# Kernel optimization log

Hardware: AMD Instinct MI355X
Metric: run time of the kernel (lower is better)

Reference implementation:

```python
import jax, jax.numpy as jnp
import numpy as np

# Model dims
B, S, H, E, I, K = 2, 2048, 1024, 8, 1024, 2
ALPHA, LIMIT = 1.702, 7.0  # gpt_oss activation constants (module defaults)


def setup_inputs() -> dict:
    key = jax.random.key(0)
    ks = jax.random.split(key, 5)
    sc = 0.02
    return {
        "hidden_states": jax.random.normal(ks[0], (B, S, H), jnp.float32),
        "router_weight": jax.random.normal(ks[1], (H, E), jnp.float32) * sc,
        "gate_up_proj": jax.random.normal(ks[2], (E, H, 2 * I), jnp.float32) * sc,
        "gate_up_proj_bias": jnp.zeros((E, 2 * I), jnp.float32),
        "down_proj": jax.random.normal(ks[3], (E, I, H), jnp.float32) * sc,
        "down_proj_bias": jnp.zeros((E, H), jnp.float32),
    }


def reference(hidden_states, router_weight, gate_up_proj, gate_up_proj_bias,
              down_proj, down_proj_bias):
    Bt, St, Ht = hidden_states.shape
    x = hidden_states.reshape(-1, Ht)           # [T, H], T = B*S
    T = x.shape[0]

    # Router: linear -> top-k -> softmax over selected logits (gpt_oss style)
    logits = x @ router_weight                  # [T, E]
    top_vals, top_idx = jax.lax.top_k(logits, K)
    scores = jax.nn.softmax(top_vals, axis=-1)  # [T, K]
    # Sparse combine weights: w[t, e] = score if e selected for t, else 0
    w = jnp.zeros((T, E), x.dtype).at[jnp.arange(T)[:, None], top_idx].set(scores)

    # Fused gate+up projection for every expert (dense equivalent of grouped GEMM;
    # unselected experts get zero combine weight so math matches sparse path)
    gu = jnp.einsum('th,ehf->tef', x, gate_up_proj) + gate_up_proj_bias  # [T, E, 2I]
    gate = gu[..., ::2]                         # interleaved gate (default)
    up = gu[..., 1::2]
    gate = jnp.minimum(gate, LIMIT)
    up = jnp.clip(up, -LIMIT, LIMIT)
    glu = gate * jax.nn.sigmoid(gate * ALPHA)
    act = (up + 1.0) * glu                      # [T, E, I]

    down = jnp.einsum('tei,eih->teh', act, down_proj) + down_proj_bias  # [T, E, H]

    # Weighted combine over experts (all-to-all combine is identity at D=1)
    out = jnp.einsum('te,teh->th', w, down)     # [T, H]
    return out.reshape(Bt, St, Ht)
```

## Files before the change

### kernel.cpp

```cpp
#include <hip/hip_runtime.h>
#include <hip/hip_bf16.h>
#include <cstdint>
#include <cstddef>

constexpr int T_TOK = 4096;
constexpr int H_DIM = 1024;
constexpr int E_NUM = 8;
constexpr int I_DIM = 1024;
constexpr int F2    = 2048;
constexpr float ALPHA = 1.702f;
constexpr float LIMIT = 7.0f;
constexpr int BM = 128;
constexpr int BK = 32;
constexpr int NT = 32;
constexpr int MAXT = 72;

using u16    = unsigned short;
using bf16x8 = __attribute__((ext_vector_type(8))) __bf16;
using s16x8  = __attribute__((ext_vector_type(8))) short;
using f32x4  = __attribute__((ext_vector_type(4))) float;

constexpr size_t WS_W1T  = 0;
constexpr size_t WS_DOWN = 0;
constexpr size_t WS_W2T  = 33554432;
constexpr size_t WS_ACT  = 50331648;
constexpr size_t WS_ETOK = 67108864;
constexpr size_t WS_POS  = 67239936;
constexpr size_t WS_CNT  = 67272704;
constexpr size_t WS_ROWB = 67272736;
constexpr size_t WS_ASGN = 67272768;
constexpr size_t WS_TOPE = 67273792;
constexpr size_t WS_TOPW = 67290176;
constexpr size_t WS_XBF  = 67322944;
constexpr size_t WS_NEED = 75711552;

__device__ __forceinline__ u16 f2bf(float f) {
    union { float f; unsigned u; } v; v.f = f;
    return (u16)((v.u + 0x7FFFu + ((v.u >> 16) & 1u)) >> 16);
}
__device__ __forceinline__ float bf2f(u16 u) {
    union { unsigned u; float f; } v; v.u = (unsigned)u << 16; return v.f;
}

__device__ __forceinline__ s16x8 pack8(float4 a, float4 b) {
    s16x8 r;
    r[0] = (short)f2bf(a.x); r[1] = (short)f2bf(a.y);
    r[2] = (short)f2bf(a.z); r[3] = (short)f2bf(a.w);
    r[4] = (short)f2bf(b.x); r[5] = (short)f2bf(b.y);
    r[6] = (short)f2bf(b.z); r[7] = (short)f2bf(b.w);
    return r;
}

__device__ __forceinline__ void gload16(const void* g, void* l) {
    __builtin_amdgcn_global_load_lds((const __attribute__((address_space(1))) unsigned*)g,
                                     (__attribute__((address_space(3))) unsigned*)l,
                                     16, 0, 0);
}

__device__ __forceinline__ void pipe_sync() {
    __builtin_amdgcn_sched_barrier(0);
    asm volatile("s_waitcnt vmcnt(0) lgkmcnt(0)" ::: "memory");
    __builtin_amdgcn_s_barrier();
    __builtin_amdgcn_sched_barrier(0);
}

__global__ __launch_bounds__(256) void k_xbf(const float* __restrict__ x,
                                             u16* __restrict__ xbf) {
    const size_t i = ((size_t)blockIdx.x * 256 + threadIdx.x) * 8;
    float4 a = *(const float4*)(x + i);
    float4 b = *(const float4*)(x + i + 4);
    *(s16x8*)(xbf + i) = pack8(a, b);
}

__global__ __launch_bounds__(256) void k_transpose_w1(const float* __restrict__ in,
                                                      u16* __restrict__ out) {
    __shared__ float tile[64][65];
    const int e = blockIdx.z, c0 = blockIdx.x * 64, h0 = blockIdx.y * 64;
    const int tid = threadIdx.x;
    const float* src = in + ((size_t)e * H_DIM + h0) * F2 + c0;
#pragma unroll
    for (int i = 0; i < 4; ++i) {
        int r = (tid >> 4) + i * 16, c = (tid & 15) * 4;
        float4 v = *(const float4*)(src + (size_t)r * F2 + c);
        tile[r][c] = v.x; tile[r][c + 1] = v.y; tile[r][c + 2] = v.z; tile[r][c + 3] = v.w;
    }
    __syncthreads();
    const int c = tid >> 2, hseg = (tid & 3) * 16;
    const int g = c & 1;
    const int f = (c0 + c) >> 1;
    u16* dst = out + (((size_t)e * 2 + g) * I_DIM + f) * H_DIM + h0 + hseg;
    s16x8 o0, o1;
#pragma unroll
    for (int j = 0; j < 8; ++j) o0[j] = (short)f2bf(tile[hseg + j][c]);
#pragma unroll
    for (int j = 0; j < 8; ++j) o1[j] = (short)f2bf(tile[hseg + 8 + j][c]);
    *(s16x8*)dst = o0;
    *(s16x8*)(dst + 8) = o1;
}

__global__ __launch_bounds__(256) void k_transpose_w2(const float* __restrict__ in,
                                                      u16* __restrict__ out) {
    __shared__ float tile[64][65];
    const int e = blockIdx.z, h0 = blockIdx.x * 64, i0 = blockIdx.y * 64;
    const int tid = threadIdx.x;
    const float* src = in + ((size_t)e * I_DIM + i0) * H_DIM + h0;
#pragma unroll
    for (int i = 0; i < 4; ++i) {
        int r = (tid >> 4) + i * 16, c = (tid & 15) * 4;
        float4 v = *(const float4*)(src + (size_t)r * H_DIM + c);
        tile[r][c] = v.x; tile[r][c + 1] = v.y; tile[r][c + 2] = v.z; tile[r][c + 3] = v.w;
    }
    __syncthreads();
    const int c = tid >> 2, iseg = (tid & 3) * 16;
    u16* dst = out + ((size_t)e * H_DIM + h0 + c) * I_DIM + i0 + iseg;
    s16x8 o0, o1;
#pragma unroll
    for (int j = 0; j < 8; ++j) o0[j] = (short)f2bf(tile[iseg + j][c]);
#pragma unroll
    for (int j = 0; j < 8; ++j) o1[j] = (short)f2bf(tile[iseg + 8 + j][c]);
    *(s16x8*)dst = o0;
    *(s16x8*)(dst + 8) = o1;
}

__global__ __launch_bounds__(256) void k_router_top2(const float* __restrict__ x,
                                                     const float* __restrict__ rw,
                                                     int* __restrict__ tope,
                                                     float2* __restrict__ topw) {
    const int wave = threadIdx.x >> 6, lane = threadIdx.x & 63;
    const int t = blockIdx.x * 4 + wave;
    const float* xr = x + (size_t)t * H_DIM;
    float acc[E_NUM];
#pragma unroll
    for (int e = 0; e < E_NUM; ++e) acc[e] = 0.f;
    for (int h = lane; h < H_DIM; h += 64) {
        float xv = xr[h];
        const float* r = rw + h * E_NUM;
#pragma unroll
        for (int e = 0; e < E_NUM; ++e) acc[e] += xv * r[e];
    }
#pragma unroll
    for (int e = 0; e < E_NUM; ++e) {
        float v = acc[e];
#pragma unroll
        for (int o = 32; o > 0; o >>= 1) v += __shfl_down(v, o);
        acc[e] = v;
    }
    if (lane == 0) {
        int e0 = 0; float v0 = acc[0];
#pragma unroll
        for (int e = 1; e < E_NUM; ++e) if (acc[e] > v0) { v0 = acc[e]; e0 = e; }
        int e1 = -1; float v1 = -3.4e38f;
#pragma unroll
        for (int e = 0; e < E_NUM; ++e) if (e != e0 && acc[e] > v1) { v1 = acc[e]; e1 = e; }
        float ew = expf(v1 - v0);
        float inv = 1.f / (1.f + ew);
        tope[t] = e0 | (e1 << 8);
        topw[t] = make_float2(inv, ew * inv);
    }
}

__global__ __launch_bounds__(256) void k_router_scatter(const int* __restrict__ tope,
                                                        int* __restrict__ cnt,
                                                        int* __restrict__ ent_tok,
                                                        int2* __restrict__ pos) {
    __shared__ int lcnt[E_NUM];
    __shared__ int gbase[E_NUM];
    const int tid = threadIdx.x;
    const int t = blockIdx.x * 256 + tid;
    if (tid < E_NUM) lcnt[tid] = 0;
    __syncthreads();
    const int pk = tope[t];
    const int e0 = pk & 0xff, e1 = pk >> 8;
    const int o0 = atomicAdd(&lcnt[e0], 1);
    const int o1 = atomicAdd(&lcnt[e1], 1);
    __syncthreads();
    if (tid < E_NUM) gbase[tid] = atomicAdd(&cnt[tid], lcnt[tid]);
    __syncthreads();
    const int p0 = gbase[e0] + o0;
    const int p1 = gbase[e1] + o1;
    ent_tok[e0 * T_TOK + p0] = t;
    ent_tok[e1 * T_TOK + p1] = t;
    pos[t] = make_int2(p0, p1);
}

__global__ void k_schedule(const int* __restrict__ cnt, int* __restrict__ rowbase,
                           int* __restrict__ assign) {
    if (threadIdx.x == 0) {
        int rb = 0, na = 0;
        for (int e = 0; e < E_NUM; ++e) {
            rowbase[e] = rb;
            int nt = (cnt[e] + BM - 1) >> 7;
            for (int m = 0; m < nt; ++m) assign[na++] = (e << 16) | m;
            rb += cnt[e];
        }
        for (; na < MAXT; ++na) assign[na] = -1;
    }
}

__global__ __launch_bounds__(256, 4) void k_gemm1(
    const u16* __restrict__ xbf, const u16* __restrict__ w1t,
    const float* __restrict__ bias, const int* __restrict__ ent_tok,
    const int* __restrict__ cnt, const int* __restrict__ rowbase,
    const int* __restrict__ assign, u16* __restrict__ act) {
    const int a = assign[blockIdx.y];
    if (a < 0) return;
    const int e = a >> 16, mt = a & 0xffff;
    const int j0 = blockIdx.x * 64;
    const int cs = cnt[e], r0 = mt * BM;
    __shared__ __align__(16) u16 As[2][BM * BK];
    __shared__ __align__(16) u16 Bs[2][BM * BK];
    const int tid = threadIdx.x, lane = tid & 63, wv = tid >> 6;
    const int lr = lane >> 2;
    const int sm = (lane & 3) ^ ((lr >> 1) & 3);
    const u16* asrc[2]; const u16* bsrc[2]; int dofs[2];
#pragma unroll
    for (int j = 0; j < 2; ++j) {
        const int row = wv * 32 + j * 16 + lr;
        const int aent = r0 + row;
        const int tok = (aent < cs) ? ent_tok[e * T_TOK + aent] : 0;
        asrc[j] = xbf + (size_t)tok * H_DIM + sm * 8;
        const int g = row >> 6;
        const int f = j0 + (row & 63);
        bsrc[j] = w1t + (((size_t)e * 2 + g) * I_DIM + f) * H_DIM + sm * 8;
        dofs[j] = (wv * 32 + j * 16) * BK;
    }
    const int wm = wv >> 1, wn = wv & 1;
    const int lcol = lane & 15, lk = lane >> 4;
    int aoff[4], goff[2], uoff[2];
#pragma unroll
    for (int mi = 0; mi < 4; ++mi) {
        const int r = wm * 64 + mi * 16 + lcol;
        aoff[mi] = r * 64 + ((lk ^ ((r >> 1) & 3)) << 4);
    }
#pragma unroll
    for (int nj = 0; nj < 2; ++nj) {
        const int rg_ = wn * 32 + nj * 16 + lcol;
        const int ru  = 64 + rg_;
        goff[nj] = rg_ * 64 + ((lk ^ ((rg_ >> 1) & 3)) << 4);
        uoff[nj] = ru  * 64 + ((lk ^ ((ru  >> 1) & 3)) << 4);
    }
    f32x4 ag[4][2], au[4][2];
    const f32x4 z = {0.f, 0.f, 0.f, 0.f};
#pragma unroll
    for (int mi = 0; mi < 4; ++mi) { ag[mi][0] = z; ag[mi][1] = z; au[mi][0] = z; au[mi][1] = z; }
#pragma unroll
    for (int j = 0; j < 2; ++j) {
        gload16(asrc[j], &As[0][dofs[j]]);
        gload16(bsrc[j], &Bs[0][dofs[j]]);
    }
    pipe_sync();
    int cur = 0;
    for (int t = 0; t < NT; ++t) {
        if (t + 1 < NT) {
            const int kn = (t + 1) * BK;
            u16* Ad = As[cur ^ 1]; u16* Bd = Bs[cur ^ 1];
#pragma unroll
            for (int j = 0; j < 2; ++j) {
                gload16(asrc[j] + kn, Ad + dofs[j]);
                gload16(bsrc[j] + kn, Bd + dofs[j]);
            }
        }
        const char* Ab = (const char*)As[cur];
        const char* Bb = (const char*)Bs[cur];
        bf16x8 af[4];
#pragma unroll
        for (int mi = 0; mi < 4; ++mi) af[mi] = *(const bf16x8*)(Ab + aoff[mi]);
        const bf16x8 g0 = *(const bf16x8*)(Bb + goff[0]);
        const bf16x8 g1 = *(const bf16x8*)(Bb + goff[1]);
        const bf16x8 u0 = *(const bf16x8*)(Bb + uoff[0]);
        const bf16x8 u1 = *(const bf16x8*)(Bb + uoff[1]);
#pragma unroll
        for (int mi = 0; mi < 4; ++mi) {
            ag[mi][0] = __builtin_amdgcn_mfma_f32_16x16x32_bf16(af[mi], g0, ag[mi][0], 0, 0, 0);
            au[mi][0] = __builtin_amdgcn_mfma_f32_16x16x32_bf16(af[mi], u0, au[mi][0], 0, 0, 0);
            ag[mi][1] = __builtin_amdgcn_mfma_f32_16x16x32_bf16(af[mi], g1, ag[mi][1], 0, 0, 0);
            au[mi][1] = __builtin_amdgcn_mfma_f32_16x16x32_bf16(af[mi], u1, au[mi][1], 0, 0, 0);
        }
        pipe_sync();
        cur ^= 1;
    }
    const int rbase = rowbase[e];
#pragma unroll
    for (int mi = 0; mi < 4; ++mi) {
#pragma unroll
        for (int nj = 0; nj < 2; ++nj) {
            const int col = j0 + wn * 32 + nj * 16 + lcol;
            const float bg_ = bias[e * F2 + 2 * col];
            const float bu_ = bias[e * F2 + 2 * col + 1];
#pragma unroll
            for (int rg = 0; rg < 4; ++rg) {
                const int r = wm * 64 + mi * 16 + lk * 4 + rg;
                if (r0 + r < cs) {
                    float gv = ag[mi][nj][rg] + bg_;
                    float uv = au[mi][nj][rg] + bu_;
                    gv = fminf(gv, LIMIT);
                    uv = fminf(fmaxf(uv, -LIMIT), LIMIT);
                    const float glu = gv / (1.f + expf(-ALPHA * gv));
                    act[(size_t)(rbase + r0 + r) * I_DIM + col] = f2bf((uv + 1.f) * glu);
                }
            }
        }
    }
}

__global__ __launch_bounds__(256, 4) void k_gemm2(
    const u16* __restrict__ act, const u16* __restrict__ w2t,
    const int* __restrict__ cnt, const int* __restrict__ rowbase,
    const int* __restrict__ assign, u16* __restrict__ down) {
    const int a = assign[blockIdx.y];
    if (a < 0) return;
    const int e = a >> 16, mt = a & 0xffff;
    const int n0 = blockIdx.x * 128;
    const int cs = cnt[e], r0 = mt * BM, rbase = rowbase[e];
    __shared__ __align__(16) u16 As[2][BM * BK];
    __shared__ __align__(16) u16 Bs[2][BM * BK];
    const int tid = threadIdx.x, lane = tid & 63, wv = tid >> 6;
    const int lr = lane >> 2;
    const int sm = (lane & 3) ^ ((lr >> 1) & 3);
    const u16* asrc[2]; const u16* bsrc[2]; int dofs[2];
#pragma unroll
    for (int j = 0; j < 2; ++j) {
        const int row = wv * 32 + j * 16 + lr;
        int ar = rbase + r0 + row;
        if (ar > 2 * T_TOK - 1) ar = 2 * T_TOK - 1;
        asrc[j] = act + (size_t)ar * I_DIM + sm * 8;
        bsrc[j] = w2t + ((size_t)e * H_DIM + n0 + row) * I_DIM + sm * 8;
        dofs[j] = (wv * 32 + j * 16) * BK;
    }
    const int wm = wv >> 1, wn = wv & 1;
    const int lcol = lane & 15, lk = lane >> 4;
    int aoff[4], boff[4];
#pragma unroll
    for (int mi = 0; mi < 4; ++mi) {
        const int r = wm * 64 + mi * 16 + lcol;
        const int b = wn * 64 + mi * 16 + lcol;
        aoff[mi] = r * 64 + ((lk ^ ((r >> 1) & 3)) << 4);
        boff[mi] = b * 64 + ((lk ^ ((b >> 1) & 3)) << 4);
    }
    f32x4 acc[4][4];
    const f32x4 z = {0.f, 0.f, 0.f, 0.f};
#pragma unroll
    for (int mi = 0; mi < 4; ++mi)
#pragma unroll
        for (int nj = 0; nj < 4; ++nj) acc[mi][nj] = z;
#pragma unroll
    for (int j = 0; j < 2; ++j) {
        gload16(asrc[j], &As[0][dofs[j]]);
        gload16(bsrc[j], &Bs[0][dofs[j]]);
    }
    pipe_sync();
    int cur = 0;
    for (int t = 0; t < NT; ++t) {
        if (t + 1 < NT) {
            const int kn = (t + 1) * BK;
            u16* Ad = As[cur ^ 1]; u16* Bd = Bs[cur ^ 1];
#pragma unroll
            for (int j = 0; j < 2; ++j) {
                gload16(asrc[j] + kn, Ad + dofs[j]);
                gload16(bsrc[j] + kn, Bd + dofs[j]);
            }
        }
        const char* Ab = (const char*)As[cur];
        const char* Bb = (const char*)Bs[cur];
        bf16x8 af[4], bf_[4];
#pragma unroll
        for (int mi = 0; mi < 4; ++mi) af[mi]  = *(const bf16x8*)(Ab + aoff[mi]);
#pragma unroll
        for (int nj = 0; nj < 4; ++nj) bf_[nj] = *(const bf16x8*)(Bb + boff[nj]);
#pragma unroll
        for (int mi = 0; mi < 4; ++mi)
#pragma unroll
            for (int nj = 0; nj < 4; ++nj)
                acc[mi][nj] = __builtin_amdgcn_mfma_f32_16x16x32_bf16(af[mi], bf_[nj], acc[mi][nj], 0, 0, 0);
        pipe_sync();
        cur ^= 1;
    }
#pragma unroll
    for (int mi = 0; mi < 4; ++mi) {
#pragma unroll
        for (int nj = 0; nj < 4; ++nj) {
            const int col = n0 + wn * 64 + nj * 16 + lcol;
#pragma unroll
            for (int rg = 0; rg < 4; ++rg) {
                const int r = wm * 64 + mi * 16 + lk * 4 + rg;
                if (r0 + r < cs)
                    down[(size_t)(rbase + r0 + r) * H_DIM + col] = f2bf(acc[mi][nj][rg]);
            }
        }
    }
}

__global__ __launch_bounds__(256) void k_combine(
    const int* __restrict__ tope, const float2* __restrict__ topw,
    const int2* __restrict__ pos, const int* __restrict__ rowb,
    const float* __restrict__ b2, const u16* __restrict__ down,
    float* __restrict__ out) {
    const int t = blockIdx.x;
    const int c = threadIdx.x * 4;
    const int pk = tope[t];
    const int e0 = pk & 0xff, e1 = pk >> 8;
    const int2 pp = pos[t];
    const float2 w = topw[t];
    const size_t ro0 = (size_t)(rowb[e0] + pp.x) * H_DIM;
    const size_t ro1 = (size_t)(rowb[e1] + pp.y) * H_DIM;
    ushort4 d0 = *(const ushort4*)(down + ro0 + c);
    ushort4 d1 = *(const ushort4*)(down + ro1 + c);
    float4 bb0 = *(const float4*)(b2 + e0 * H_DIM + c);
    float4 bb1 = *(const float4*)(b2 + e1 * H_DIM + c);
    float4 o;
    o.x = w.x * (bf2f(d0.x) + bb0.x) + w.y * (bf2f(d1.x) + bb1.x);
    o.y = w.x * (bf2f(d0.y) + bb0.y) + w.y * (bf2f(d1.y) + bb1.y);
    o.z = w.x * (bf2f(d0.z) + bb0.z) + w.y * (bf2f(d1.z) + bb1.z);
    o.w = w.x * (bf2f(d0.w) + bb0.w) + w.y * (bf2f(d1.w) + bb1.w);
    *(float4*)(out + (size_t)t * H_DIM + c) = o;
}

extern "C" void kernel_launch(void* const* d_in, const int* in_sizes, int n_in,
                              void* d_out, int out_size, void* d_ws, size_t ws_size,
                              hipStream_t stream) {
    const float* x   = (const float*)d_in[0];
    const float* rw  = (const float*)d_in[1];
    const float* w1  = (const float*)d_in[2];
    const float* b1  = (const float*)d_in[3];
    const float* w2  = (const float*)d_in[4];
    const float* b2  = (const float*)d_in[5];
    float* out = (float*)d_out;
    char* ws = (char*)d_ws;

    if (ws_size < WS_NEED) return;

    u16*    W1T  = (u16*)(ws + WS_W1T);
    u16*    DOWN = (u16*)(ws + WS_DOWN);
    u16*    W2T  = (u16*)(ws + WS_W2T);
    u16*    ACT  = (u16*)(ws + WS_ACT);
    int*    ETOK = (int*)(ws + WS_ETOK);
    int2*   POS  = (int2*)(ws + WS_POS);
    int*    CNT  = (int*)(ws + WS_CNT);
    int*    ROWB = (int*)(ws + WS_ROWB);
    int*    ASGN = (int*)(ws + WS_ASGN);
    int*    TOPE = (int*)(ws + WS_TOPE);
    float2* TOPW = (float2*)(ws + WS_TOPW);
    u16*    XBF  = (u16*)(ws + WS_XBF);

    hipMemsetAsync(CNT, 0, E_NUM * sizeof(int), stream);

    k_xbf<<<T_TOK * H_DIM / 2048, 256, 0, stream>>>(x, XBF);
    k_transpose_w1<<<dim3(32, 16, 8), 256, 0, stream>>>(w1, W1T);
    k_transpose_w2<<<dim3(16, 16, 8), 256, 0, stream>>>(w2, W2T);
    k_router_top2<<<T_TOK / 4, 256, 0, stream>>>(x, rw, TOPE, TOPW);
    k_router_scatter<<<T_TOK / 256, 256, 0, stream>>>(TOPE, CNT, ETOK, POS);
    k_schedule<<<1, 64, 0, stream>>>(CNT, ROWB, ASGN);
    k_gemm1<<<dim3(16, MAXT), 256, 0, stream>>>(XBF, W1T, b1, ETOK, CNT, ROWB, ASGN, ACT);
    k_gemm2<<<dim3(8, MAXT), 256, 0, stream>>>(ACT, W2T, CNT, ROWB, ASGN, DOWN);
    k_combine<<<T_TOK, 256, 0, stream>>>(TOPE, TOPW, POS, ROWB, b2, DOWN, out);
}
```

Before: 165.2 us.

## Grow GEMM M-tile to 256 rows with 512-thread blocks sharing B tile

Doubles the M tile of both grouped GEMMs from 128 to 256 rows and launches 8 waves per block. The B (weight) tile stays at 128 rows, loaded once per k-step by all eight waves and shared across both M halves. This halves the number of times each weight tile is fetched per expert and cuts the tile count (MAXT 72 to 40). In exchange, padding waste for partially filled experts grows, there are fewer blocks to fill the GPU, and shared memory per block rises.

Result: slower. 170.7 us (+3.3%).

```diff
diff --git a/kernel.cpp b/kernel.cpp
--- a/kernel.cpp
+++ b/kernel.cpp
@@ -10,10 +10,10 @@
 constexpr int F2    = 2048;
 constexpr float ALPHA = 1.702f;
 constexpr float LIMIT = 7.0f;
-constexpr int BM = 128;
+constexpr int BM = 256;
 constexpr int BK = 32;
 constexpr int NT = 32;
-constexpr int MAXT = 72;
+constexpr int MAXT = 40;
 
 using u16    = unsigned short;
 using bf16x8 = __attribute__((ext_vector_type(8))) __bf16;
@@ -189,7 +189,7 @@
         int rb = 0, na = 0;
         for (int e = 0; e < E_NUM; ++e) {
             rowbase[e] = rb;
-            int nt = (cnt[e] + BM - 1) >> 7;
+            int nt = (cnt[e] + BM - 1) >> 8;
             for (int m = 0; m < nt; ++m) assign[na++] = (e << 16) | m;
             rb += cnt[e];
         }
@@ -197,7 +197,7 @@
     }
 }
 
-__global__ __launch_bounds__(256, 4) void k_gemm1(
+__global__ __launch_bounds__(512, 4) void k_gemm1(
     const u16* __restrict__ xbf, const u16* __restrict__ w1t,
     const float* __restrict__ bias, const int* __restrict__ ent_tok,
     const int* __restrict__ cnt, const int* __restrict__ rowbase,
@@ -208,22 +208,24 @@
     const int j0 = blockIdx.x * 64;
     const int cs = cnt[e], r0 = mt * BM;
     __shared__ __align__(16) u16 As[2][BM * BK];
-    __shared__ __align__(16) u16 Bs[2][BM * BK];
+    __shared__ __align__(16) u16 Bs[2][128 * BK];
     const int tid = threadIdx.x, lane = tid & 63, wv = tid >> 6;
     const int lr = lane >> 2;
     const int sm = (lane & 3) ^ ((lr >> 1) & 3);
-    const u16* asrc[2]; const u16* bsrc[2]; int dofs[2];
+    const u16* asrc[2]; int dofsA[2];
 #pragma unroll
     for (int j = 0; j < 2; ++j) {
         const int row = wv * 32 + j * 16 + lr;
         const int aent = r0 + row;
         const int tok = (aent < cs) ? ent_tok[e * T_TOK + aent] : 0;
         asrc[j] = xbf + (size_t)tok * H_DIM + sm * 8;
-        const int g = row >> 6;
-        const int f = j0 + (row & 63);
-        bsrc[j] = w1t + (((size_t)e * 2 + g) * I_DIM + f) * H_DIM + sm * 8;
-        dofs[j] = (wv * 32 + j * 16) * BK;
-    }
+        dofsA[j] = (wv * 32 + j * 16) * BK;
+    }
+    const int brow = wv * 16 + lr;
+    const int bg = brow >> 6;
+    const int bf = j0 + (brow & 63);
+    const u16* bsrc = w1t + (((size_t)e * 2 + bg) * I_DIM + bf) * H_DIM + sm * 8;
+    const int dofsB = (wv * 16) * BK;
     const int wm = wv >> 1, wn = wv & 1;
     const int lcol = lane & 15, lk = lane >> 4;
     int aoff[4], goff[2], uoff[2];
@@ -244,10 +246,8 @@
 #pragma unroll
     for (int mi = 0; mi < 4; ++mi) { ag[mi][0] = z; ag[mi][1] = z; au[mi][0] = z; au[mi][1] = z; }
 #pragma unroll
-    for (int j = 0; j < 2; ++j) {
-        gload16(asrc[j], &As[0][dofs[j]]);
-        gload16(bsrc[j], &Bs[0][dofs[j]]);
-    }
+    for (int j = 0; j < 2; ++j) gload16(asrc[j], &As[0][dofsA[j]]);
+    gload16(bsrc, &Bs[0][dofsB]);
     pipe_sync();
     int cur = 0;
     for (int t = 0; t < NT; ++t) {
@@ -255,10 +255,8 @@
             const int kn = (t + 1) * BK;
             u16* Ad = As[cur ^ 1]; u16* Bd = Bs[cur ^ 1];
 #pragma unroll
-            for (int j = 0; j < 2; ++j) {
-                gload16(asrc[j] + kn, Ad + dofs[j]);
-                gload16(bsrc[j] + kn, Bd + dofs[j]);
-            }
+            for (int j = 0; j < 2; ++j) gload16(asrc[j] + kn, Ad + dofsA[j]);
+            gload16(bsrc + kn, Bd + dofsB);
         }
         const char* Ab = (const char*)As[cur];
         const char* Bb = (const char*)Bs[cur];
@@ -303,8 +301,8 @@
     }
 }
 
-__global__ __launch_bounds__(256, 4) void k_gemm2(
-    const u16* __restrict__ act, const u16* __restrict__ w2t,
+__global__ __launch_bounds__(512, 4) void k_gemm2(
+    const u16* __restrict__ actb, const u16* __restrict__ w2t,
     const int* __restrict__ cnt, const int* __restrict__ rowbase,
     const int* __restrict__ assign, u16* __restrict__ down) {
     const int a = assign[blockIdx.y];
@@ -313,29 +311,34 @@
     const int n0 = blockIdx.x * 128;
     const int cs = cnt[e], r0 = mt * BM, rbase = rowbase[e];
     __shared__ __align__(16) u16 As[2][BM * BK];
-    __shared__ __align__(16) u16 Bs[2][BM * BK];
+    __shared__ __align__(16) u16 Bs[2][128 * BK];
     const int tid = threadIdx.x, lane = tid & 63, wv = tid >> 6;
     const int lr = lane >> 2;
     const int sm = (lane & 3) ^ ((lr >> 1) & 3);
-    const u16* asrc[2]; const u16* bsrc[2]; int dofs[2];
+    const u16* asrc[2]; int dofsA[2];
 #pragma unroll
     for (int j = 0; j < 2; ++j) {
         const int row = wv * 32 + j * 16 + lr;
         int ar = rbase + r0 + row;
         if (ar > 2 * T_TOK - 1) ar = 2 * T_TOK - 1;
-        asrc[j] = act + (size_t)ar * I_DIM + sm * 8;
-        bsrc[j] = w2t + ((size_t)e * H_DIM + n0 + row) * I_DIM + sm * 8;
-        dofs[j] = (wv * 32 + j * 16) * BK;
-    }
+        asrc[j] = actb + (size_t)ar * I_DIM + sm * 8;
+        dofsA[j] = (wv * 32 + j * 16) * BK;
+    }
+    const int brow = wv * 16 + lr;
+    const u16* bsrc = w2t + ((size_t)e * H_DIM + n0 + brow) * I_DIM + sm * 8;
+    const int dofsB = (wv * 16) * BK;
     const int wm = wv >> 1, wn = wv & 1;
     const int lcol = lane & 15, lk = lane >> 4;
     int aoff[4], boff[4];
 #pragma unroll
     for (int mi = 0; mi < 4; ++mi) {
         const int r = wm * 64 + mi * 16 + lcol;
-        const int b = wn * 64 + mi * 16 + lcol;
         aoff[mi] = r * 64 + ((lk ^ ((r >> 1) & 3)) << 4);
-        boff[mi] = b * 64 + ((lk ^ ((b >> 1) & 3)) << 4);
+    }
+#pragma unroll
+    for (int nj = 0; nj < 4; ++nj) {
+        const int b = wn * 64 + nj * 16 + lcol;
+        boff[nj] = b * 64 + ((lk ^ ((b >> 1) & 3)) << 4);
     }
     f32x4 acc[4][4];
     const f32x4 z = {0.f, 0.f, 0.f, 0.f};
@@ -344,10 +347,8 @@
 #pragma unroll
         for (int nj = 0; nj < 4; ++nj) acc[mi][nj] = z;
 #pragma unroll
-    for (int j = 0; j < 2; ++j) {
-        gload16(asrc[j], &As[0][dofs[j]]);
-        gload16(bsrc[j], &Bs[0][dofs[j]]);
-    }
+    for (int j = 0; j < 2; ++j) gload16(asrc[j], &As[0][dofsA[j]]);
+    gload16(bsrc, &Bs[0][dofsB]);
     pipe_sync();
     int cur = 0;
     for (int t = 0; t < NT; ++t) {
@@ -355,10 +356,8 @@
             const int kn = (t + 1) * BK;
             u16* Ad = As[cur ^ 1]; u16* Bd = Bs[cur ^ 1];
 #pragma unroll
-            for (int j = 0; j < 2; ++j) {
-                gload16(asrc[j] + kn, Ad + dofs[j]);
-                gload16(bsrc[j] + kn, Bd + dofs[j]);
-            }
+            for (int j = 0; j < 2; ++j) gload16(asrc[j] + kn, Ad + dofsA[j]);
+            gload16(bsrc + kn, Bd + dofsB);
         }
         const char* Ab = (const char*)As[cur];
         const char* Bb = (const char*)Bs[cur];
@@ -450,7 +449,7 @@
     k_router_top2<<<T_TOK / 4, 256, 0, stream>>>(x, rw, TOPE, TOPW);
     k_router_scatter<<<T_TOK / 256, 256, 0, stream>>>(TOPE, CNT, ETOK, POS);
     k_schedule<<<1, 64, 0, stream>>>(CNT, ROWB, ASGN);
-    k_gemm1<<<dim3(16, MAXT), 256, 0, stream>>>(XBF, W1T, b1, ETOK, CNT, ROWB, ASGN, ACT);
-    k_gemm2<<<dim3(8, MAXT), 256, 0, stream>>>(ACT, W2T, CNT, ROWB, ASGN, DOWN);
+    k_gemm1<<<dim3(16, MAXT), 512, 0, stream>>>(XBF, W1T, b1, ETOK, CNT, ROWB, ASGN, ACT);
+    k_gemm2<<<dim3(8, MAXT), 512, 0, stream>>>(ACT, W2T, CNT, ROWB, ASGN, DOWN);
     k_combine<<<T_TOK, 256, 0, stream>>>(TOPE, TOPW, POS, ROWB, b2, DOWN, out);
 }
```
